# Optimization experiments

Hardware: AMD Instinct MI355X
Metric: run time of the kernel (lower is better)

The kernel has to match this reference:

```python
import jax, jax.numpy as jnp
import numpy as np

# near_sym_b (13,19)-tap biorthogonal level-1 DTCWT filters (Kingsbury)
H0O = np.array([-0.0017578125, 0.0, 0.022265625, -0.046875, -0.0482421875,
                0.296875, 0.5554687500, 0.296875, -0.0482421875, -0.046875,
                0.022265625, 0.0, -0.0017578125], dtype=np.float32)
H1O = np.array([-7.0626e-05, 0.0, 1.34189e-03, -1.88341e-03, -7.15660e-03,
                2.38560e-02, 5.56431e-02, -5.16881e-02, -2.99758e-01,
                5.59431e-01, -2.99758e-01, -5.16881e-02, 5.56431e-02,
                2.38560e-02, -7.15660e-03, -1.88341e-03, 1.34189e-03,
                0.0, -7.0626e-05], dtype=np.float32)

def _alt(h):
    c = (len(h) - 1) // 2
    return (h * ((-1.0) ** (np.arange(len(h)) - c))).astype(np.float32)

G0O = _alt(H1O)  # synthesis lowpass  (PR complement of H1O)
G1O = _alt(H0O)  # synthesis highpass (PR complement of H0O)

DIM, HS, WS, BATCH, NB, BS = 64, 56, 56, 32, 4, 16


def _filt(x, h, axis):
    # depthwise 1D correlation with symmetric padding; x: (B,C,H,W), axis in {2,3}
    L = len(h); p = L // 2
    pad = [(0, 0)] * 4; pad[axis] = (p, p)
    xp = jnp.pad(x, pad, mode='symmetric')
    k = jnp.asarray(h, x.dtype).reshape((1, 1, L, 1) if axis == 2 else (1, 1, 1, L))
    B, C = x.shape[:2]
    y = jax.lax.conv_general_dilated(
        xp.reshape((B * C, 1) + xp.shape[2:]), k, (1, 1), 'VALID',
        dimension_numbers=('NCHW', 'OIHW', 'NCHW'))
    return y.reshape((B, C) + y.shape[2:])


def _q2c(y):
    y = y * np.float32(1.0 / np.sqrt(2.0))
    a = y[..., 0::2, 0::2]; b = y[..., 0::2, 1::2]
    c = y[..., 1::2, 0::2]; d = y[..., 1::2, 1::2]
    return (a - d, b + c), (a + d, b - c)


def _c2q(w1r, w1i, w2r, w2i):
    sc = np.float32(1.0 / np.sqrt(2.0))
    B, C, Hh, Wh = w1r.shape
    top = jnp.stack([(w1r + w2r) * sc, (w1i + w2i) * sc], axis=-1).reshape(B, C, Hh, 2 * Wh)
    bot = jnp.stack([(w1i - w2i) * sc, (w2r - w1r) * sc], axis=-1).reshape(B, C, Hh, 2 * Wh)
    return jnp.stack([top, bot], axis=3).reshape(B, C, 2 * Hh, 2 * Wh)


def dtcwt_fwd_j1(x):
    lo = _filt(x, H0O, 3); hi = _filt(x, H1O, 3)
    ll = _filt(lo, H0O, 2)
    (d15r, d15i), (d165r, d165i) = _q2c(_filt(lo, H1O, 2))   # LH -> 15/165 deg
    (d75r, d75i), (d105r, d105i) = _q2c(_filt(hi, H0O, 2))   # HL -> 75/105 deg
    (d45r, d45i), (d135r, d135i) = _q2c(_filt(hi, H1O, 2))   # HH -> 45/135 deg
    real = jnp.stack([d15r, d45r, d75r, d105r, d135r, d165r], axis=2)
    imag = jnp.stack([d15i, d45i, d75i, d105i, d135i, d165i], axis=2)
    return ll, jnp.stack([real, imag], axis=-1)  # (B,C,H,W), (B,C,6,H/2,W/2,2)


def dtcwt_inv_j1(ll, yh):
    r = yh[..., 0]; im = yh[..., 1]
    lh = _c2q(r[:, :, 0], im[:, :, 0], r[:, :, 5], im[:, :, 5])
    hl = _c2q(r[:, :, 2], im[:, :, 2], r[:, :, 3], im[:, :, 3])
    hh = _c2q(r[:, :, 1], im[:, :, 1], r[:, :, 4], im[:, :, 4])
    lo = _filt(ll, G0O, 2) + _filt(lh, G1O, 2)
    hi = _filt(hl, G0O, 2) + _filt(hh, G1O, 2)
    return _filt(lo, G0O, 3) + _filt(hi, G1O, 3)


def setup_inputs():
    key = jax.random.key(0)
    ks = jax.random.split(key, 6)
    return {
        'x': jax.random.normal(ks[0], (BATCH, HS * WS, DIM), jnp.float32),
        'w_ll': jax.random.normal(ks[1], (DIM, HS, WS), jnp.float32) * 0.02,
        'w1': jax.random.normal(ks[2], (2, NB, BS, BS), jnp.float32) * 0.02,
        'w2': jax.random.normal(ks[3], (2, NB, BS, BS), jnp.float32) * 0.02,
        'b1': jax.random.normal(ks[4], (2, NB, BS), jnp.float32) * 0.02,
        'b2': jax.random.normal(ks[5], (2, NB, BS), jnp.float32) * 0.02,
        'H': HS, 'W': WS,
    }


def reference(x, w_ll, w1, w2, b1, b2, H, W):
    Bt, N, C = x.shape
    xi = jnp.transpose(x.reshape(Bt, H, W, C), (0, 3, 1, 2)).astype(jnp.float32)
    xl, xh = dtcwt_fwd_j1(xi)
    xl = xl * w_ll                                  # (B,C,H,W) * (C,H,W)
    Hh, Wh = H // 2, W // 2
    # (B,C,6,Hh,Wh,2) -> (2,B,6,Hh,Wh,C) -> split C into (NB,BS) blocks
    xh = jnp.transpose(xh, (5, 0, 2, 3, 4, 1)).reshape(2, Bt, 6, Hh, Wh, NB, BS)
    xr, xim = xh[0], xh[1]
    mul = lambda t, w: jnp.einsum('...bd,bdk->...bk', t, w)
    r1 = jax.nn.relu(mul(xr, w1[0]) - mul(xim, w1[1]) + b1[0])
    i1 = jax.nn.relu(mul(xr, w1[1]) + mul(xim, w1[0]) + b1[1])
    r2 = mul(r1, w2[0]) - mul(i1, w2[1]) + b2[0]
    i2 = mul(r1, w2[1]) + mul(i1, w2[0]) + b2[1]
    xh2 = jnp.stack([r2, i2], axis=-1).reshape(Bt, 6, Hh, Wh, C, 2)
    xh2 = jnp.transpose(xh2, (0, 4, 1, 2, 3, 5))    # (B,C,6,Hh,Wh,2)
    y = dtcwt_inv_j1(xl, xh2)
    return jnp.transpose(y, (0, 2, 3, 1)).reshape(Bt, N, C)
```

## Files before the change

### kernel.cpp

```cpp
#include <hip/hip_runtime.h>

#define BT 32
#define CH 64
#define HS 56
#define WS 56
#define HH 28
#define WH 28

namespace {
constexpr float ISQ2 = 0.70710678118654752440f;
constexpr float F_H0[13] = {-0.0017578125f, 0.0f, 0.022265625f, -0.046875f,
    -0.0482421875f, 0.296875f, 0.55546875f, 0.296875f, -0.0482421875f,
    -0.046875f, 0.022265625f, 0.0f, -0.0017578125f};
constexpr float F_H1[19] = {-7.0626e-05f, 0.0f, 0.00134189f, -0.00188341f,
    -0.0071566f, 0.023856f, 0.0556431f, -0.0516881f, -0.299758f, 0.559431f,
    -0.299758f, -0.0516881f, 0.0556431f, 0.023856f, -0.0071566f,
    -0.00188341f, 0.00134189f, 0.0f, -7.0626e-05f};
constexpr float F_G0[19] = {7.0626e-05f, 0.0f, -0.00134189f, -0.00188341f,
    0.0071566f, 0.023856f, -0.0556431f, -0.0516881f, 0.299758f, 0.559431f,
    0.299758f, -0.0516881f, -0.0556431f, 0.023856f, 0.0071566f,
    -0.00188341f, -0.00134189f, 0.0f, 7.0626e-05f};
constexpr float F_G1[13] = {-0.0017578125f, 0.0f, 0.022265625f, 0.046875f,
    -0.0482421875f, -0.296875f, 0.55546875f, -0.296875f, -0.0482421875f,
    0.046875f, 0.022265625f, 0.0f, -0.0017578125f};
}

__device__ __forceinline__ int symi(int k) {
    k = (k < 0) ? (-1 - k) : k;
    k = (k >= HS) ? (2 * HS - 1 - k) : k;
    return k;
}

__device__ __forceinline__ unsigned short f2bf(float f) {
    unsigned u = __float_as_uint(f);
    u += 0x7fffu + ((u >> 16) & 1u);
    return (unsigned short)(u >> 16);
}
__device__ __forceinline__ float bf2f(unsigned short h) {
    return __uint_as_float(((unsigned)h) << 16);
}
__device__ __forceinline__ float2 bfp2(unsigned u) {
    float2 r;
    r.x = __uint_as_float((u & 0xffffu) << 16);
    r.y = __uint_as_float(u & 0xffff0000u);
    return r;
}
__device__ __forceinline__ unsigned packbf(float a, float b) {
    return (unsigned)f2bf(a) | ((unsigned)f2bf(b) << 16);
}

typedef __attribute__((ext_vector_type(8))) short short8;
typedef __attribute__((ext_vector_type(4))) float f32x4;

#define PPOS 784

__global__ __launch_bounds__(256) void k_wll_T(const float* __restrict__ wll,
                                               float* __restrict__ wllT) {
    __shared__ float tile[64][65];
    int pos0 = blockIdx.x * 64;
    int lp = threadIdx.x & 63, g = threadIdx.x >> 6;
#pragma unroll
    for (int r = 0; r < 16; ++r) {
        int cc = r * 4 + g;
        tile[cc][lp] = wll[cc * (HS * WS) + pos0 + lp];
    }
    __syncthreads();
#pragma unroll
    for (int r = 0; r < 16; ++r) {
        int pl = r * 4 + g;
        wllT[(pos0 + pl) * CH + lp] = tile[lp][pl];
    }
}

__global__ __launch_bounds__(256) void k_fwd_rows(const float* __restrict__ x,
                                                  unsigned short* __restrict__ lo,
                                                  unsigned short* __restrict__ hi) {
    int b = blockIdx.x / HS, h = blockIdx.x % HS;
    int strip = threadIdx.x >> 5;
    int c0 = (threadIdx.x & 31) * 2;
    int base = (b * HS + h) * WS * CH + c0;
    const float* row = x + base;
    unsigned short* lop = lo + base;
    unsigned short* hip = hi + base;
    int w0s = strip * 7;
    float Wa[19], Wb[19];
#pragma unroll
    for (int t = 0; t < 19; ++t) {
        float2 v = *(const float2*)(row + symi(w0s - 9 + t) * CH);
        Wa[t] = v.x; Wb[t] = v.y;
    }
    float2 nW[7];
#pragma unroll
    for (int u = 0; u < 7; ++u) nW[u] = *(const float2*)(row + symi(w0s + u + 10) * CH);
#pragma unroll
    for (int u = 0; u < 7; ++u) {
        int w = w0s + u;
        float aLo = 0.f, aHi = 0.f, bLo = 0.f, bHi = 0.f;
#pragma unroll
        for (int t = 0; t < 13; ++t) { aLo += F_H0[t] * Wa[3 + t]; bLo += F_H0[t] * Wb[3 + t]; }
#pragma unroll
        for (int t = 0; t < 19; ++t) { aHi += F_H1[t] * Wa[t]; bHi += F_H1[t] * Wb[t]; }
        *(unsigned*)(lop + w * CH) = packbf(aLo, bLo);
        *(unsigned*)(hip + w * CH) = packbf(aHi, bHi);
#pragma unroll
        for (int t = 0; t < 18; ++t) { Wa[t] = Wa[t + 1]; Wb[t] = Wb[t + 1]; }
        Wa[18] = nW[u].x; Wb[18] = nW[u].y;
    }
}

__global__ __launch_bounds__(256) void k_cols(
    const unsigned short* __restrict__ lo_in,
    const unsigned short* __restrict__ hi_in, const float* __restrict__ wllT,
    float* __restrict__ xl, unsigned short* __restrict__ sbT) {
    __shared__ float qT[2][4][64][15];
    int hf = blockIdx.y;
    int zmode = blockIdx.z;
    int b = blockIdx.x / WH, wp = blockIdx.x % WH;
    int w0 = 2 * wp, tid = threadIdx.x;
    int q = tid >> 6, c = tid & 63;
    int rp = q >> 1, jc = q & 1;
    const unsigned short* srcp = zmode ? hi_in : lo_in;
    const unsigned short* colbase = srcp + (b * HS) * WS * CH + (w0 + jc) * CH + c;
    {
        int hstart = 2 * (hf * 14) + rp;
        float W[19];
#pragma unroll
        for (int t = 0; t < 19; ++t) W[t] = bf2f(colbase[symi(hstart - 9 + t) * (WS * CH)]);
        float nW0[14], nW1[14], nwll[14];
#pragma unroll
        for (int u = 0; u < 14; ++u) {
            int h = hstart + 2 * u;
            nW0[u] = bf2f(colbase[symi(h + 10) * (WS * CH)]);
            nW1[u] = bf2f(colbase[symi(h + 11) * (WS * CH)]);
        }
        if (zmode == 0) {
#pragma unroll
            for (int u = 0; u < 14; ++u)
                nwll[u] = wllT[((hstart + 2 * u) * WS + (w0 + jc)) * CH + c];
        }
#pragma unroll
        for (int u = 0; u < 14; ++u) {
            int h = hstart + 2 * u;
            float v0 = 0.f, v1 = 0.f;
#pragma unroll
            for (int t = 0; t < 13; ++t) v0 += F_H0[t] * W[3 + t];
#pragma unroll
            for (int t = 0; t < 19; ++t) v1 += F_H1[t] * W[t];
            if (zmode == 0) {
                xl[((b * HS + h) * WS + (w0 + jc)) * CH + c] = v0 * nwll[u];
                qT[0][q][c][u] = v1;
            } else {
                qT[0][q][c][u] = v0;
                qT[1][q][c][u] = v1;
            }
#pragma unroll
            for (int t = 0; t < 17; ++t) W[t] = W[t + 2];
            W[17] = nW0[u];
            W[18] = nW1[u];
        }
    }
    __syncthreads();
    {
        int qq = tid >> 5;
        int role = qq & 3, half = qq >> 2;
        int c0 = (tid & 31) * 2;
        int rowA = role & 1, rowB = 3 - (role & 1);
        float sgn = (role == 1 || role == 2) ? 1.f : -1.f;
        int posb = wp * 28 + hf * 14;
        if (zmode == 0) {
            int p = (role < 2) ? role : role + 8;
            const float* qA0 = &qT[0][rowA][c0][0];
            const float* qA1 = &qT[0][rowA][c0 + 1][0];
            const float* qB0 = &qT[0][rowB][c0][0];
            const float* qB1 = &qT[0][rowB][c0 + 1][0];
            unsigned short* dst = sbT + ((p * BT + b) * PPOS + posb) * CH + c0;
#pragma unroll
            for (int g = 0; g < 7; ++g) {
                int ii = half * 7 + g;
                float v0 = (qA0[ii] + sgn * qB0[ii]) * ISQ2;
                float v1 = (qA1[ii] + sgn * qB1[ii]) * ISQ2;
                *(unsigned*)(dst + ii * CH) = packbf(v0, v1);
            }
        } else {
#pragma unroll
            for (int src = 0; src < 2; ++src) {
                int p = (src == 0) ? (4 + role) : ((role < 2) ? (2 + role) : (6 + role));
                const float* qA0 = &qT[src][rowA][c0][0];
                const float* qA1 = &qT[src][rowA][c0 + 1][0];
                const float* qB0 = &qT[src][rowB][c0][0];
                const float* qB1 = &qT[src][rowB][c0 + 1][0];
                unsigned short* dst = sbT + ((p * BT + b) * PPOS + posb) * CH + c0;
#pragma unroll
                for (int g = 0; g < 7; ++g) {
                    int ii = half * 7 + g;
                    float v0 = (qA0[ii] + sgn * qB0[ii]) * ISQ2;
                    float v1 = (qA1[ii] + sgn * qB1[ii]) * ISQ2;
                    *(unsigned*)(dst + ii * CH) = packbf(v0, v1);
                }
            }
        }
    }
}

__global__ __launch_bounds__(256) void k_mix(
    const unsigned short* __restrict__ sbT, const float* __restrict__ w1,
    const float* __restrict__ w2, const float* __restrict__ b1,
    const float* __restrict__ b2, unsigned short* __restrict__ P0,
    unsigned short* __restrict__ P1, unsigned short* __restrict__ P2) {
    __shared__ unsigned short l1a[4][16][36];
    __shared__ unsigned short l1b[4][16][36];
    int blk = blockIdx.x;
    int pr = blk / (BT * 7);
    int rem = blk % (BT * 7);
    int b = rem / 7;
    int chunk = rem % 7;
    int sa = (pr == 0) ? 0 : (pr == 1) ? 2 : 1;
    int sb = (pr == 0) ? 5 : (pr == 1) ? 3 : 4;
    unsigned short* Pd = (pr == 0) ? P0 : (pr == 1) ? P1 : P2;
    int tid = threadIdx.x;
    int lane = tid & 63;
    int wv = tid >> 6;
    int nb = __builtin_amdgcn_readfirstlane(wv);
    int quad = lane >> 4;
    int n = lane & 15;

    short8 B1r, B1i, B2r, B2i;
#pragma unroll
    for (int j = 0; j < 8; ++j) {
        int kk = quad * 8 + j;
        int riw = kk >> 4, dd = kk & 15;
        float v1r = w1[nb * 256 + dd * 16 + n];
        float v1i = w1[1024 + nb * 256 + dd * 16 + n];
        float v2r = w2[nb * 256 + dd * 16 + n];
        float v2i = w2[1024 + nb * 256 + dd * 16 + n];
        B1r[j] = (short)f2bf(riw ? -v1i : v1r);
        B1i[j] = (short)f2bf(riw ? v1r : v1i);
        B2r[j] = (short)f2bf(riw ? -v2i : v2r);
        B2i[j] = (short)f2bf(riw ? v2r : v2i);
    }
    float bias1r = b1[nb * 16 + n], bias1i = b1[64 + nb * 16 + n];
    float bias2r = b2[nb * 16 + n], bias2i = b2[64 + nb * 16 + n];

    int rix = quad >> 1, dlo = (quad & 1) * 8;
    const unsigned short* pAa =
        sbT + (((sa * 2 + rix) * BT + b) * PPOS + n) * CH + nb * 16 + dlo;
    const unsigned short* pAb =
        sbT + (((sb * 2 + rix) * BT + b) * PPOS + n) * CH + nb * 16 + dlo;

    int pbase = chunk * 112;
    short8 A1a = *(const short8*)(pAa + pbase * CH);
    short8 A1b = *(const short8*)(pAb + pbase * CH);
    for (int t = 0; t < 7; ++t) {
        int pos0 = pbase + t * 16;
        short8 nAa = A1a, nAb = A1b;
        if (t < 6) {
            nAa = *(const short8*)(pAa + (pos0 + 16) * CH);
            nAb = *(const short8*)(pAb + (pos0 + 16) * CH);
        }
        f32x4 a1r = {bias1r, bias1r, bias1r, bias1r};
        f32x4 a1i = {bias1i, bias1i, bias1i, bias1i};
        f32x4 b1r_ = a1r, b1i_ = a1i;
        a1r = __builtin_amdgcn_mfma_f32_16x16x32_bf16(A1a, B1r, a1r, 0, 0, 0);
        a1i = __builtin_amdgcn_mfma_f32_16x16x32_bf16(A1a, B1i, a1i, 0, 0, 0);
        b1r_ = __builtin_amdgcn_mfma_f32_16x16x32_bf16(A1b, B1r, b1r_, 0, 0, 0);
        b1i_ = __builtin_amdgcn_mfma_f32_16x16x32_bf16(A1b, B1i, b1i_, 0, 0, 0);
#pragma unroll
        for (int r = 0; r < 4; ++r) {
            int pos = quad * 4 + r;
            l1a[wv][pos][n] = f2bf(fmaxf(a1r[r], 0.f));
            l1a[wv][pos][16 + n] = f2bf(fmaxf(a1i[r], 0.f));
            l1b[wv][pos][n] = f2bf(fmaxf(b1r_[r], 0.f));
            l1b[wv][pos][16 + n] = f2bf(fmaxf(b1i_[r], 0.f));
        }
        union { short8 s8; uint2 u2[2]; } a2a, a2b;
        const unsigned short* rowpa = &l1a[wv][n][0];
        const unsigned short* rowpb = &l1b[wv][n][0];
        a2a.u2[0] = *(const uint2*)(rowpa + quad * 8);
        a2a.u2[1] = *(const uint2*)(rowpa + quad * 8 + 4);
        a2b.u2[0] = *(const uint2*)(rowpb + quad * 8);
        a2b.u2[1] = *(const uint2*)(rowpb + quad * 8 + 4);
        f32x4 aAr = {bias2r, bias2r, bias2r, bias2r};
        f32x4 aAi = {bias2i, bias2i, bias2i, bias2i};
        f32x4 aBr = aAr, aBi = aAi;
        aAr = __builtin_amdgcn_mfma_f32_16x16x32_bf16(a2a.s8, B2r, aAr, 0, 0, 0);
        aAi = __builtin_amdgcn_mfma_f32_16x16x32_bf16(a2a.s8, B2i, aAi, 0, 0, 0);
        aBr = __builtin_amdgcn_mfma_f32_16x16x32_bf16(a2b.s8, B2r, aBr, 0, 0, 0);
        aBi = __builtin_amdgcn_mfma_f32_16x16x32_bf16(a2b.s8, B2i, aBi, 0, 0, 0);
#pragma unroll
        for (int r = 0; r < 4; ++r) {
            int pos_g = pos0 + quad * 4 + r;
            int wp = pos_g / 28, ii = pos_g - wp * 28;
            int o = ((b * HS + 2 * ii) * WS + 2 * wp) * CH + nb * 16 + n;
            Pd[o] = f2bf((aAr[r] + aBr[r]) * ISQ2);
            Pd[o + CH] = f2bf((aAi[r] + aBi[r]) * ISQ2);
            Pd[o + WS * CH] = f2bf((aAi[r] - aBi[r]) * ISQ2);
            Pd[o + WS * CH + CH] = f2bf((aBr[r] - aAr[r]) * ISQ2);
        }
        A1a = nAa; A1b = nAb;
    }
}

template <int MODE>
__device__ __forceinline__ void inv_cols_body(
    const float* __restrict__ xl, const unsigned short* __restrict__ P0,
    const unsigned short* __restrict__ P1, const unsigned short* __restrict__ P2,
    float* __restrict__ lo2, float* __restrict__ hi2) {
    int hf = blockIdx.y;
    int b = blockIdx.x / 7, wg = blockIdx.x % 7;
    int wl = threadIdx.x >> 5, l = threadIdx.x & 31;
    int c0 = l * 2;
    int w = wg * 8 + wl;
    int base = (b * HS) * WS * CH + w * CH + c0;
    const int st = WS * CH;
    const unsigned short* Bp = (MODE == 0) ? P0 : P2;
    float* outp = (MODE == 0) ? lo2 : hi2;
    auto ldA = [&](int r) -> float2 {
        if (MODE == 0) return *(const float2*)(xl + base + r * st);
        return bfp2(*(const unsigned*)(P1 + base + r * st));
    };
    auto ldB = [&](int r) -> float2 {
        return bfp2(*(const unsigned*)(Bp + base + r * st));
    };
    int h0 = hf * 28;
    float Aa[19], Ab[19], Ba[13], Bb[13];
#pragma unroll
    for (int t = 0; t < 19; ++t) { float2 v = ldA(symi(h0 - 9 + t)); Aa[t] = v.x; Ab[t] = v.y; }
#pragma unroll
    for (int t = 0; t < 13; ++t) { float2 v = ldB(symi(h0 - 6 + t)); Ba[t] = v.x; Bb[t] = v.y; }
    float2 pa0[4], pb0[4], pa1[4], pb1[4];
#define LDG(bA, bB, G)                                                          \
    {                                                                           \
        _Pragma("unroll") for (int u = 0; u < 4; ++u)                           \
            bA[u] = ldA(symi(h0 + (G) * 4 + u + 10));                           \
        _Pragma("unroll") for (int u = 0; u < 4; ++u)                           \
            bB[u] = ldB(symi(h0 + (G) * 4 + u + 7));                            \
    }
#define CPG(bA, bB, G)                                                          \
    {                                                                           \
        _Pragma("unroll") for (int u = 0; u < 4; ++u) {                         \
            int h = h0 + (G) * 4 + u;                                           \
            float acca = 0.f, accb = 0.f;                                       \
            _Pragma("unroll") for (int t = 0; t < 19; ++t) {                    \
                acca += F_G0[t] * Aa[t]; accb += F_G0[t] * Ab[t];               \
            }                                                                   \
            _Pragma("unroll") for (int t = 0; t < 13; ++t) {                    \
                acca += F_G1[t] * Ba[t]; accb += F_G1[t] * Bb[t];               \
            }                                                                   \
            float2 ov; ov.x = acca; ov.y = accb;                                \
            *(float2*)(outp + base + h * st) = ov;                              \
            _Pragma("unroll") for (int t = 0; t < 18; ++t) {                    \
                Aa[t] = Aa[t + 1]; Ab[t] = Ab[t + 1];                           \
            }                                                                   \
            _Pragma("unroll") for (int t = 0; t < 12; ++t) {                    \
                Ba[t] = Ba[t + 1]; Bb[t] = Bb[t + 1];                           \
            }                                                                   \
            Aa[18] = bA[u].x; Ab[18] = bA[u].y;                                 \
            Ba[12] = bB[u].x; Bb[12] = bB[u].y;                                 \
        }                                                                       \
    }
    LDG(pa0, pb0, 0) LDG(pa1, pb1, 1)
    CPG(pa0, pb0, 0) LDG(pa0, pb0, 2)
    CPG(pa1, pb1, 1) LDG(pa1, pb1, 3)
    CPG(pa0, pb0, 2) LDG(pa0, pb0, 4)
    CPG(pa1, pb1, 3) LDG(pa1, pb1, 5)
    CPG(pa0, pb0, 4) LDG(pa0, pb0, 6)
    CPG(pa1, pb1, 5)
    CPG(pa0, pb0, 6)
#undef LDG
#undef CPG
}

__global__ __launch_bounds__(256) void k_inv_cols(
    const float* __restrict__ xl, const unsigned short* __restrict__ P0,
    const unsigned short* __restrict__ P1, const unsigned short* __restrict__ P2,
    float* __restrict__ lo2, float* __restrict__ hi2) {
    if (blockIdx.z == 0)
        inv_cols_body<0>(xl, P0, P1, P2, lo2, hi2);
    else
        inv_cols_body<1>(xl, P0, P1, P2, lo2, hi2);
}

__global__ __launch_bounds__(256) void k_inv_rows(const float* __restrict__ lo2,
                                                  const float* __restrict__ hi2,
                                                  float* __restrict__ out) {
    int b = blockIdx.x / HS, h = blockIdx.x % HS;
    int strip = threadIdx.x >> 5;
    int c0 = (threadIdx.x & 31) * 2;
    int base = (b * HS + h) * WS * CH + c0;
    const float* rlo = lo2 + base;
    const float* rhi = hi2 + base;
    float* op = out + base;
    int w0s = strip * 7;
    float Aa[19], Ab[19], Ba[13], Bb[13];
#pragma unroll
    for (int t = 0; t < 19; ++t) {
        float2 v = *(const float2*)(rlo + symi(w0s - 9 + t) * CH);
        Aa[t] = v.x; Ab[t] = v.y;
    }
#pragma unroll
    for (int t = 0; t < 13; ++t) {
        float2 v = *(const float2*)(rhi + symi(w0s - 6 + t) * CH);
        Ba[t] = v.x; Bb[t] = v.y;
    }
    float2 nA[7], nB[7];
#pragma unroll
    for (int u = 0; u < 7; ++u) nA[u] = *(const float2*)(rlo + symi(w0s + u + 10) * CH);
#pragma unroll
    for (int u = 0; u < 7; ++u) nB[u] = *(const float2*)(rhi + symi(w0s + u + 7) * CH);
#pragma unroll
    for (int u = 0; u < 7; ++u) {
        int w = w0s + u;
        float acca = 0.f, accb = 0.f;
#pragma unroll
        for (int t = 0; t < 19; ++t) { acca += F_G0[t] * Aa[t]; accb += F_G0[t] * Ab[t]; }
#pragma unroll
        for (int t = 0; t < 13; ++t) { acca += F_G1[t] * Ba[t]; accb += F_G1[t] * Bb[t]; }
        float2 ov; ov.x = acca; ov.y = accb;
        *(float2*)(op + w * CH) = ov;
#pragma unroll
        for (int t = 0; t < 18; ++t) { Aa[t] = Aa[t + 1]; Ab[t] = Ab[t + 1]; }
#pragma unroll
        for (int t = 0; t < 12; ++t) { Ba[t] = Ba[t + 1]; Bb[t] = Bb[t + 1]; }
        Aa[18] = nA[u].x; Ab[18] = nA[u].y;
        Ba[12] = nB[u].x; Bb[12] = nB[u].y;
    }
}

extern "C" void kernel_launch(void* const* d_in, const int* in_sizes, int n_in,
                              void* d_out, int out_size, void* d_ws, size_t ws_size,
                              hipStream_t stream) {
    const float* x = (const float*)d_in[0];
    const float* w_ll = (const float*)d_in[1];
    const float* w1 = (const float*)d_in[2];
    const float* w2 = (const float*)d_in[3];
    const float* b1 = (const float*)d_in[4];
    const float* b2 = (const float*)d_in[5];
    float* out = (float*)d_out;

    const size_t A = (size_t)BT * HS * WS * CH;
    const size_t SBf = (size_t)12 * 64 * BT * PPOS / 2;
    float* wsf = (float*)d_ws;
    float* xl = wsf;
    unsigned short* sbT = (unsigned short*)(wsf + A);
    float* lo2 = wsf + A;
    float* hi2 = wsf + A + SBf;
    unsigned short* lo_in = (unsigned short*)(wsf + A + SBf + A);
    unsigned short* hi_in = lo_in + A;
    unsigned short* P0 = hi_in + A;
    unsigned short* P1 = P0 + A;
    unsigned short* P2 = P1 + A;

    float* wllT = out;

    k_wll_T<<<49, 256, 0, stream>>>(w_ll, wllT);
    k_fwd_rows<<<BT * HS, 256, 0, stream>>>(x, lo_in, hi_in);
    k_cols<<<dim3(BT * WH, 2, 2), 256, 0, stream>>>(lo_in, hi_in, wllT, xl, sbT);
    k_mix<<<3 * BT * 7, 256, 0, stream>>>(sbT, w1, w2, b1, b2, P0, P1, P2);
    k_inv_cols<<<dim3(BT * 7, 2, 2), 256, 0, stream>>>(xl, P0, P1, P2, lo2, hi2);
    k_inv_rows<<<BT * HS, 256, 0, stream>>>(lo2, hi2, out);
}
```

Measured before the change: 178.6 us.

## Fuse column forward transform with complex channel mixing via shared memory

Merges the column-filter kernel and the MFMA channel-mix kernel into one kernel. The 12 subband slices for a 14-position tile stay in LDS and are fed straight into the MFMA mix, so the bf16 sbT intermediate is no longer written to and read back from global memory and one launch goes away. In exchange each block processes both lo and hi sources serially, with more syncs, half the blocks, and MFMA tiles padded from 14 to 16 rows, which leaves some lanes idle.

```diff
diff --git a/kernel.cpp b/kernel.cpp
--- a/kernel.cpp
+++ b/kernel.cpp
@@ -108,121 +108,29 @@
     }
 }
 
-__global__ __launch_bounds__(256) void k_cols(
+__global__ __launch_bounds__(256) void k_cols_mix(
     const unsigned short* __restrict__ lo_in,
     const unsigned short* __restrict__ hi_in, const float* __restrict__ wllT,
-    float* __restrict__ xl, unsigned short* __restrict__ sbT) {
-    __shared__ float qT[2][4][64][15];
+    const float* __restrict__ w1, const float* __restrict__ w2,
+    const float* __restrict__ b1, const float* __restrict__ b2,
+    float* __restrict__ xl, unsigned short* __restrict__ P0,
+    unsigned short* __restrict__ P1, unsigned short* __restrict__ P2) {
+    __shared__ __align__(16) char smem0[2 * 4 * 64 * 9 * 4];
+    __shared__ __align__(16) unsigned short pA[12][16][72];
+    float (*qT)[4][64][9] = (float(*)[4][64][9])smem0;
+    unsigned short (*l1a)[16][36] = (unsigned short(*)[16][36])smem0;
+    unsigned short (*l1b)[16][36] =
+        (unsigned short(*)[16][36])(smem0 + 4 * 16 * 36 * 2);
+
     int hf = blockIdx.y;
-    int zmode = blockIdx.z;
     int b = blockIdx.x / WH, wp = blockIdx.x % WH;
     int w0 = 2 * wp, tid = threadIdx.x;
     int q = tid >> 6, c = tid & 63;
     int rp = q >> 1, jc = q & 1;
-    const unsigned short* srcp = zmode ? hi_in : lo_in;
-    const unsigned short* colbase = srcp + (b * HS) * WS * CH + (w0 + jc) * CH + c;
-    {
-        int hstart = 2 * (hf * 14) + rp;
-        float W[19];
-#pragma unroll
-        for (int t = 0; t < 19; ++t) W[t] = bf2f(colbase[symi(hstart - 9 + t) * (WS * CH)]);
-        float nW0[14], nW1[14], nwll[14];
-#pragma unroll
-        for (int u = 0; u < 14; ++u) {
-            int h = hstart + 2 * u;
-            nW0[u] = bf2f(colbase[symi(h + 10) * (WS * CH)]);
-            nW1[u] = bf2f(colbase[symi(h + 11) * (WS * CH)]);
-        }
-        if (zmode == 0) {
-#pragma unroll
-            for (int u = 0; u < 14; ++u)
-                nwll[u] = wllT[((hstart + 2 * u) * WS + (w0 + jc)) * CH + c];
-        }
-#pragma unroll
-        for (int u = 0; u < 14; ++u) {
-            int h = hstart + 2 * u;
-            float v0 = 0.f, v1 = 0.f;
-#pragma unroll
-            for (int t = 0; t < 13; ++t) v0 += F_H0[t] * W[3 + t];
-#pragma unroll
-            for (int t = 0; t < 19; ++t) v1 += F_H1[t] * W[t];
-            if (zmode == 0) {
-                xl[((b * HS + h) * WS + (w0 + jc)) * CH + c] = v0 * nwll[u];
-                qT[0][q][c][u] = v1;
-            } else {
-                qT[0][q][c][u] = v0;
-                qT[1][q][c][u] = v1;
-            }
-#pragma unroll
-            for (int t = 0; t < 17; ++t) W[t] = W[t + 2];
-            W[17] = nW0[u];
-            W[18] = nW1[u];
-        }
-    }
-    __syncthreads();
-    {
-        int qq = tid >> 5;
-        int role = qq & 3, half = qq >> 2;
-        int c0 = (tid & 31) * 2;
-        int rowA = role & 1, rowB = 3 - (role & 1);
-        float sgn = (role == 1 || role == 2) ? 1.f : -1.f;
-        int posb = wp * 28 + hf * 14;
-        if (zmode == 0) {
-            int p = (role < 2) ? role : role + 8;
-            const float* qA0 = &qT[0][rowA][c0][0];
-            const float* qA1 = &qT[0][rowA][c0 + 1][0];
-            const float* qB0 = &qT[0][rowB][c0][0];
-            const float* qB1 = &qT[0][rowB][c0 + 1][0];
-            unsigned short* dst = sbT + ((p * BT + b) * PPOS + posb) * CH + c0;
-#pragma unroll
-            for (int g = 0; g < 7; ++g) {
-                int ii = half * 7 + g;
-                float v0 = (qA0[ii] + sgn * qB0[ii]) * ISQ2;
-                float v1 = (qA1[ii] + sgn * qB1[ii]) * ISQ2;
-                *(unsigned*)(dst + ii * CH) = packbf(v0, v1);
-            }
-        } else {
-#pragma unroll
-            for (int src = 0; src < 2; ++src) {
-                int p = (src == 0) ? (4 + role) : ((role < 2) ? (2 + role) : (6 + role));
-                const float* qA0 = &qT[src][rowA][c0][0];
-                const float* qA1 = &qT[src][rowA][c0 + 1][0];
-                const float* qB0 = &qT[src][rowB][c0][0];
-                const float* qB1 = &qT[src][rowB][c0 + 1][0];
-                unsigned short* dst = sbT + ((p * BT + b) * PPOS + posb) * CH + c0;
-#pragma unroll
-                for (int g = 0; g < 7; ++g) {
-                    int ii = half * 7 + g;
-                    float v0 = (qA0[ii] + sgn * qB0[ii]) * ISQ2;
-                    float v1 = (qA1[ii] + sgn * qB1[ii]) * ISQ2;
-                    *(unsigned*)(dst + ii * CH) = packbf(v0, v1);
-                }
-            }
-        }
-    }
-}
-
-__global__ __launch_bounds__(256) void k_mix(
-    const unsigned short* __restrict__ sbT, const float* __restrict__ w1,
-    const float* __restrict__ w2, const float* __restrict__ b1,
-    const float* __restrict__ b2, unsigned short* __restrict__ P0,
-    unsigned short* __restrict__ P1, unsigned short* __restrict__ P2) {
-    __shared__ unsigned short l1a[4][16][36];
-    __shared__ unsigned short l1b[4][16][36];
-    int blk = blockIdx.x;
-    int pr = blk / (BT * 7);
-    int rem = blk % (BT * 7);
-    int b = rem / 7;
-    int chunk = rem % 7;
-    int sa = (pr == 0) ? 0 : (pr == 1) ? 2 : 1;
-    int sb = (pr == 0) ? 5 : (pr == 1) ? 3 : 4;
-    unsigned short* Pd = (pr == 0) ? P0 : (pr == 1) ? P1 : P2;
-    int tid = threadIdx.x;
     int lane = tid & 63;
     int wv = tid >> 6;
+    int quad = lane >> 4, n = lane & 15;
     int nb = __builtin_amdgcn_readfirstlane(wv);
-    int quad = lane >> 4;
-    int n = lane & 15;
 
     short8 B1r, B1i, B2r, B2i;
 #pragma unroll
@@ -241,22 +149,90 @@
     float bias1r = b1[nb * 16 + n], bias1i = b1[64 + nb * 16 + n];
     float bias2r = b2[nb * 16 + n], bias2i = b2[64 + nb * 16 + n];
 
+    for (int src = 0; src < 2; ++src) {
+        const unsigned short* srcp = src ? hi_in : lo_in;
+        const unsigned short* colbase =
+            srcp + (b * HS) * WS * CH + (w0 + jc) * CH + c;
+        int hstart = 2 * (hf * 14) + rp;
+        float W[19];
+#pragma unroll
+        for (int t = 0; t < 19; ++t)
+            W[t] = bf2f(colbase[symi(hstart - 9 + t) * (WS * CH)]);
+        float nW0[14], nW1[14], nwll[14];
+#pragma unroll
+        for (int u = 0; u < 14; ++u) {
+            int h = hstart + 2 * u;
+            nW0[u] = bf2f(colbase[symi(h + 10) * (WS * CH)]);
+            nW1[u] = bf2f(colbase[symi(h + 11) * (WS * CH)]);
+        }
+        if (src == 0) {
+#pragma unroll
+            for (int u = 0; u < 14; ++u)
+                nwll[u] = wllT[((hstart + 2 * u) * WS + (w0 + jc)) * CH + c];
+        }
+        for (int rnd = 0; rnd < 2; ++rnd) {
+#pragma unroll
+            for (int g = 0; g < 7; ++g) {
+                int u = rnd * 7 + g;
+                int h = hstart + 2 * u;
+                float v0 = 0.f, v1 = 0.f;
+#pragma unroll
+                for (int t = 0; t < 13; ++t) v0 += F_H0[t] * W[3 + t];
+#pragma unroll
+                for (int t = 0; t < 19; ++t) v1 += F_H1[t] * W[t];
+                if (src == 0) {
+                    xl[((b * HS + h) * WS + (w0 + jc)) * CH + c] = v0 * nwll[u];
+                    qT[0][q][c][g] = v1;
+                } else {
+                    qT[0][q][c][g] = v0;
+                    qT[1][q][c][g] = v1;
+                }
+#pragma unroll
+                for (int t = 0; t < 17; ++t) W[t] = W[t + 2];
+                W[17] = nW0[u];
+                W[18] = nW1[u];
+            }
+            __syncthreads();
+            {
+                int qq = tid >> 5;
+                int role = qq & 3, sub = qq >> 2;
+                int c0 = (tid & 31) * 2;
+                int rowA = role & 1, rowB = 3 - (role & 1);
+                float sgn = (role == 1 || role == 2) ? 1.f : -1.f;
+                int iL = sub ? 4 : 0, iH = sub ? 7 : 4;
+                if (src == 0) {
+                    int p = (role < 2) ? role : role + 8;
+                    for (int ii = iL; ii < iH; ++ii) {
+                        float v0 = (qT[0][rowA][c0][ii] + sgn * qT[0][rowB][c0][ii]) * ISQ2;
+                        float v1 = (qT[0][rowA][c0 + 1][ii] + sgn * qT[0][rowB][c0 + 1][ii]) * ISQ2;
+                        *(unsigned*)&pA[p][rnd * 7 + ii][c0] = packbf(v0, v1);
+                    }
+                } else {
+#pragma unroll
+                    for (int s2 = 0; s2 < 2; ++s2) {
+                        int p = (s2 == 0) ? (4 + role)
+                                          : ((role < 2) ? (2 + role) : (6 + role));
+                        for (int ii = iL; ii < iH; ++ii) {
+                            float v0 = (qT[s2][rowA][c0][ii] + sgn * qT[s2][rowB][c0][ii]) * ISQ2;
+                            float v1 = (qT[s2][rowA][c0 + 1][ii] + sgn * qT[s2][rowB][c0 + 1][ii]) * ISQ2;
+                            *(unsigned*)&pA[p][rnd * 7 + ii][c0] = packbf(v0, v1);
+                        }
+                    }
+                }
+            }
+            __syncthreads();
+        }
+    }
+
     int rix = quad >> 1, dlo = (quad & 1) * 8;
-    const unsigned short* pAa =
-        sbT + (((sa * 2 + rix) * BT + b) * PPOS + n) * CH + nb * 16 + dlo;
-    const unsigned short* pAb =
-        sbT + (((sb * 2 + rix) * BT + b) * PPOS + n) * CH + nb * 16 + dlo;
-
-    int pbase = chunk * 112;
-    short8 A1a = *(const short8*)(pAa + pbase * CH);
-    short8 A1b = *(const short8*)(pAb + pbase * CH);
-    for (int t = 0; t < 7; ++t) {
-        int pos0 = pbase + t * 16;
-        short8 nAa = A1a, nAb = A1b;
-        if (t < 6) {
-            nAa = *(const short8*)(pAa + (pos0 + 16) * CH);
-            nAb = *(const short8*)(pAb + (pos0 + 16) * CH);
-        }
+    int chb = nb * 16 + dlo;
+#pragma unroll
+    for (int pr = 0; pr < 3; ++pr) {
+        const int sa = (pr == 0) ? 0 : (pr == 1) ? 2 : 1;
+        const int sb = (pr == 0) ? 5 : (pr == 1) ? 3 : 4;
+        unsigned short* Pd = (pr == 0) ? P0 : (pr == 1) ? P1 : P2;
+        short8 A1a = *(const short8*)&pA[sa * 2 + rix][n][chb];
+        short8 A1b = *(const short8*)&pA[sb * 2 + rix][n][chb];
         f32x4 a1r = {bias1r, bias1r, bias1r, bias1r};
         f32x4 a1i = {bias1i, bias1i, bias1i, bias1i};
         f32x4 b1r_ = a1r, b1i_ = a1i;
@@ -288,15 +264,16 @@
         aBi = __builtin_amdgcn_mfma_f32_16x16x32_bf16(a2b.s8, B2i, aBi, 0, 0, 0);
 #pragma unroll
         for (int r = 0; r < 4; ++r) {
-            int pos_g = pos0 + quad * 4 + r;
-            int wp = pos_g / 28, ii = pos_g - wp * 28;
-            int o = ((b * HS + 2 * ii) * WS + 2 * wp) * CH + nb * 16 + n;
-            Pd[o] = f2bf((aAr[r] + aBr[r]) * ISQ2);
-            Pd[o + CH] = f2bf((aAi[r] + aBi[r]) * ISQ2);
-            Pd[o + WS * CH] = f2bf((aAi[r] - aBi[r]) * ISQ2);
-            Pd[o + WS * CH + CH] = f2bf((aBr[r] - aAr[r]) * ISQ2);
+            int m = quad * 4 + r;
+            if (m < 14) {
+                int iimg = hf * 14 + m;
+                int o = ((b * HS + 2 * iimg) * WS + 2 * wp) * CH + nb * 16 + n;
+                Pd[o] = f2bf((aAr[r] + aBr[r]) * ISQ2);
+                Pd[o + CH] = f2bf((aAi[r] + aBi[r]) * ISQ2);
+                Pd[o + WS * CH] = f2bf((aAi[r] - aBi[r]) * ISQ2);
+                Pd[o + WS * CH + CH] = f2bf((aBr[r] - aAr[r]) * ISQ2);
+            }
         }
-        A1a = nAa; A1b = nAb;
     }
 }
 
@@ -441,7 +418,6 @@
     const size_t SBf = (size_t)12 * 64 * BT * PPOS / 2;
     float* wsf = (float*)d_ws;
     float* xl = wsf;
-    unsigned short* sbT = (unsigned short*)(wsf + A);
     float* lo2 = wsf + A;
     float* hi2 = wsf + A + SBf;
     unsigned short* lo_in = (unsigned short*)(wsf + A + SBf + A);
@@ -454,8 +430,8 @@
 
     k_wll_T<<<49, 256, 0, stream>>>(w_ll, wllT);
     k_fwd_rows<<<BT * HS, 256, 0, stream>>>(x, lo_in, hi_in);
-    k_cols<<<dim3(BT * WH, 2, 2), 256, 0, stream>>>(lo_in, hi_in, wllT, xl, sbT);
-    k_mix<<<3 * BT * 7, 256, 0, stream>>>(sbT, w1, w2, b1, b2, P0, P1, P2);
+    k_cols_mix<<<dim3(BT * WH, 2), 256, 0, stream>>>(lo_in, hi_in, wllT, w1, w2,
+                                                     b1, b2, xl, P0, P1, P2);
     k_inv_cols<<<dim3(BT * 7, 2, 2), 256, 0, stream>>>(xl, P0, P1, P2, lo2, hi2);
     k_inv_rows<<<BT * HS, 256, 0, stream>>>(lo2, hi2, out);
 }
```

Measured after the change: 218.9 us. 1.23x slower.
